# Performance work log

Measured on AMD Instinct MI355X. Metric: run time of the kernel, lower is better.

The kernel has to match this reference:

```python
import jax, jax.numpy as jnp
import numpy as np

B = 4; D = H = W = 28; C = 192; NH = 6; WS = 7; SS = 3
L = D * H * W; N = WS ** 3; HD = C // NH


def _rel_index():
    c = np.stack(np.meshgrid(np.arange(WS), np.arange(WS), np.arange(WS), indexing='ij')).reshape(3, -1)
    r = c[:, :, None] - c[:, None, :] + (WS - 1)
    return jnp.asarray(r[0] * (2 * WS - 1) ** 2 + r[1] * (2 * WS - 1) + r[2])  # (N,N)


def _attn_mask():
    img = np.zeros((D, H, W), np.float32)
    sl = (slice(0, -WS), slice(-WS, -SS), slice(-SS, None))
    cnt = 0
    for d in sl:
        for h in sl:
            for w in sl:
                img[d, h, w] = cnt; cnt += 1
    mw = img.reshape(D // WS, WS, H // WS, WS, W // WS, WS).transpose(0, 2, 4, 1, 3, 5).reshape(-1, N)
    am = mw[:, None, :] - mw[:, :, None]
    return jnp.asarray(np.where(am != 0, -100.0, 0.0).astype(np.float32))  # (nW,N,N)

REL_IDX = _rel_index()
ATTN_MASK = _attn_mask()


def _ln(x, g, b):
    m = x.mean(-1, keepdims=True)
    v = ((x - m) ** 2).mean(-1, keepdims=True)
    return (x - m) / jnp.sqrt(v + 1e-5) * g + b


def _window_partition(x):  # (B,D,H,W,C) -> (B*nW, N, C)
    x = x.reshape(B, D // WS, WS, H // WS, WS, W // WS, WS, C)
    return x.transpose(0, 1, 3, 5, 2, 4, 6, 7).reshape(-1, N, C)


def _window_reverse(w):  # (B*nW, N, C) -> (B,D,H,W,C)
    x = w.reshape(B, D // WS, H // WS, W // WS, WS, WS, WS, C)
    return x.transpose(0, 1, 4, 2, 5, 3, 6, 7).reshape(B, D, H, W, C)


def setup_inputs() -> dict:
    key = jax.random.key(0)
    ks = jax.random.split(key, 8)
    s = 0.02
    return {
        'x': jax.random.normal(ks[0], (B, L, C), jnp.float32),
        'norm1_g': jnp.ones((C,), jnp.float32), 'norm1_b': jnp.zeros((C,), jnp.float32),
        'qkv_w': jax.random.normal(ks[1], (3 * C, C), jnp.float32) * s,
        'qkv_b': jnp.zeros((3 * C,), jnp.float32),
        'proj_w': jax.random.normal(ks[2], (C, C), jnp.float32) * s,
        'proj_b': jnp.zeros((C,), jnp.float32),
        'rel_table': jax.random.normal(ks[3], ((2 * WS - 1) ** 3, NH), jnp.float32) * s,
        'norm2_g': jnp.ones((C,), jnp.float32), 'norm2_b': jnp.zeros((C,), jnp.float32),
        'fc1_w': jax.random.normal(ks[4], (4 * C, C), jnp.float32) * s,
        'fc1_b': jnp.zeros((4 * C,), jnp.float32),
        'fc2_w': jax.random.normal(ks[5], (C, 4 * C), jnp.float32) * s,
        'fc2_b': jnp.zeros((C,), jnp.float32),
    }


def reference(x, norm1_g, norm1_b, qkv_w, qkv_b, proj_w, proj_b, rel_table,
              norm2_g, norm2_b, fc1_w, fc1_b, fc2_w, fc2_b):
    shortcut = x
    h = _ln(x, norm1_g, norm1_b).reshape(B, D, H, W, C)
    h = jnp.roll(h, (-SS, -SS, -SS), axis=(1, 2, 3))
    xw = _window_partition(h)                                  # (B_, N, C)
    B_ = xw.shape[0]
    qkv = (xw @ qkv_w.T + qkv_b).reshape(B_, N, 3, NH, HD).transpose(2, 0, 3, 1, 4)
    q, k, v = qkv[0], qkv[1], qkv[2]                           # (B_, NH, N, HD)
    attn = jnp.einsum('bhnd,bhmd->bhnm', q * (HD ** -0.5), k)
    bias = rel_table[REL_IDX].transpose(2, 0, 1)               # (NH, N, N)
    attn = attn + bias[None]
    nW = ATTN_MASK.shape[0]
    attn = (attn.reshape(B, nW, NH, N, N) + ATTN_MASK[None, :, None]).reshape(B_, NH, N, N)
    attn = jax.nn.softmax(attn, axis=-1)
    out = jnp.einsum('bhnm,bhmd->bhnd', attn, v).transpose(0, 2, 1, 3).reshape(B_, N, C)
    out = out @ proj_w.T + proj_b
    h = _window_reverse(out)
    h = jnp.roll(h, (SS, SS, SS), axis=(1, 2, 3)).reshape(B, L, C)
    x = shortcut + h
    y = _ln(x, norm2_g, norm2_b)
    y = jax.nn.gelu(y @ fc1_w.T + fc1_b, approximate=False)
    return x + (y @ fc2_w.T + fc2_b)
```

## Files before the change

kernel.cpp:

```cpp
#include <hip/hip_runtime.h>

#define DEV __device__ __forceinline__

typedef __bf16 bf16x8 __attribute__((ext_vector_type(8)));
typedef float f32x4 __attribute__((ext_vector_type(4)));

DEV float bflo(unsigned int u) { union { unsigned int x; float f; } c; c.x = u << 16; return c.f; }
DEV unsigned short f2bf(float f) {
  union { float f; unsigned int u; } c; c.f = f;
  unsigned int u = c.u;
  return (unsigned short)((u + 0x7fffu + ((u >> 16) & 1u)) >> 16);
}
DEV unsigned int pkbf(float a, float b) {
  unsigned int r;
  asm("v_cvt_pk_bf16_f32 %0, %1, %2" : "=v"(r) : "v"(a), "v"(b));
  return r;
}
DEV float gelu_fast(float y) {
  float y2 = y * y;
  float z = y * fmaf(y2, 0.10294348f, 2.30220842f);
  float e = __builtin_amdgcn_exp2f(z);
  float r = __builtin_amdgcn_rcpf(e + 1.0f);
  return fmaf(-y, r, y);
}

DEV void gload16(const void* g, void* l) {
  __builtin_amdgcn_global_load_lds((const __attribute__((address_space(1))) void*)g,
                                   (__attribute__((address_space(3))) void*)l, 16, 0, 0);
}

__global__ __launch_bounds__(256) void wconv_all(const float* __restrict__ s0,
                                                 const float* __restrict__ s1,
                                                 const float* __restrict__ s2,
                                                 const float* __restrict__ s3,
                                                 unsigned short* __restrict__ dst) {
  int i = blockIdx.x * 256 + threadIdx.x;
  const float* src; int off, real;
  if (i < 122880)      { src = s0; off = i;          real = 110592; }
  else if (i < 172032) { src = s1; off = i - 122880; real = 36864; }
  else if (i < 319488) { src = s2; off = i - 172032; real = 147456; }
  else                 { src = s3; off = i - 319488; real = 147456; }
  dst[i] = (off < real) ? f2bf(src[off]) : (unsigned short)0;
}

__global__ __launch_bounds__(256) void bmt_kernel(const float* __restrict__ rel_table,
                                                  unsigned short* __restrict__ bmt4) {
  int wth = blockIdx.x;
  int wt = wth / 6, h = wth - wt * 6;
  int r = blockIdx.y;
  unsigned short* row = bmt4 + (((size_t)wth * 88 + r) * 352) * 4;
  for (int q = threadIdx.x; q < 352; q += 256) {
    int mb_q = 0, cls_q = 0;
    bool qv = q < 343;
    if (qv) {
      int ii_q = q / 49, rem_q = q - ii_q * 49;
      int jj_q = rem_q / 7, ww_q = rem_q - jj_q * 7;
      mb_q = ii_q * 169 + jj_q * 13 + ww_q;
      int cd_q = (wt & 4) ? (ii_q < 4 ? 1 : 2) : 0;
      int ch_q = (wt & 2) ? (jj_q < 4 ? 1 : 2) : 0;
      int cw_q = (wt & 1) ? (ww_q < 4 ? 1 : 2) : 0;
      cls_q = cd_q * 9 + ch_q * 3 + cw_q;
    }
    unsigned short ov[4];
#pragma unroll
    for (int i = 0; i < 4; i++) {
      int kk = 4 * r + i;
      float v;
      if (kk >= 343) v = -30000.f;
      else if (!qv) v = 0.f;
      else {
        int ii_k = kk / 49, rem_k = kk - ii_k * 49;
        int jj_k = rem_k / 7, ww_k = rem_k - jj_k * 7;
        int mb_k = ii_k * 169 + jj_k * 13 + ww_k;
        int cd_k = (wt & 4) ? (ii_k < 4 ? 1 : 2) : 0;
        int ch_k = (wt & 2) ? (jj_k < 4 ? 1 : 2) : 0;
        int cw_k = (wt & 1) ? (ww_k < 4 ? 1 : 2) : 0;
        int cls_k = cd_k * 9 + ch_k * 3 + cw_k;
        v = rel_table[(mb_q - mb_k + 1098) * 6 + h] * 1.4426950408889634f;
        if (cls_q != cls_k) v -= 144.26950408889634f;
      }
      ov[i] = f2bf(v);
    }
    unsigned int lo = (unsigned)ov[0] | ((unsigned)ov[1] << 16);
    unsigned int hi = (unsigned)ov[2] | ((unsigned)ov[3] << 16);
    *(uint2*)(row + q * 4) = make_uint2(lo, hi);
  }
}

__global__ __launch_bounds__(256) void ln_kernel(const float* __restrict__ x,
                                                 const float* __restrict__ g,
                                                 const float* __restrict__ b,
                                                 unsigned short* __restrict__ out) {
  int row = (blockIdx.x << 2) + (threadIdx.x >> 6);
  int lane = threadIdx.x & 63;
  int w_ = row / 343, n_ = row - w_ * 343;
  int bb = w_ >> 6, wrem = w_ & 63;
  int wd = wrem >> 4, wh = (wrem >> 2) & 3, ww = wrem & 3;
  int ii = n_ / 49, rem = n_ - ii * 49;
  int jj = rem / 7, kk = rem - jj * 7;
  int d = wd * 7 + ii + 3; if (d >= 28) d -= 28;
  int hh = wh * 7 + jj + 3; if (hh >= 28) hh -= 28;
  int wb = ww * 7 + kk + 3; if (wb >= 28) wb -= 28;
  const float* xr = x + ((size_t)bb * 21952 + (d * 28 + hh) * 28 + wb) * 192;
  float v0 = xr[lane], v1 = xr[lane + 64], v2 = xr[lane + 128];
  float s = v0 + v1 + v2;
  float sq = v0 * v0 + v1 * v1 + v2 * v2;
#pragma unroll
  for (int o = 32; o > 0; o >>= 1) {
    s += __shfl_xor(s, o, 64);
    sq += __shfl_xor(sq, o, 64);
  }
  float mean = s * (1.0f / 192.0f);
  float var = sq * (1.0f / 192.0f) - mean * mean;
  float rstd = rsqrtf(var + 1e-5f);
  unsigned short* orow = out + (size_t)row * 192;
  orow[lane]       = f2bf((v0 - mean) * rstd * g[lane] + b[lane]);
  orow[lane + 64]  = f2bf((v1 - mean) * rstd * g[lane + 64] + b[lane + 64]);
  orow[lane + 128] = f2bf((v2 - mean) * rstd * g[lane + 128] + b[lane + 128]);
}

__global__ __launch_bounds__(256) void gemm_qkv(
    const unsigned short* __restrict__ A, const unsigned short* __restrict__ W,
    const float* __restrict__ bias,
    unsigned short* __restrict__ oq, unsigned short* __restrict__ okk,
    unsigned short* __restrict__ ov) {
  __shared__ __align__(16) unsigned short As[2][128 * 64];
  __shared__ __align__(16) unsigned short Bs[2][128 * 64];
  const int K = 192;
  const int orig = blockIdx.x;
  const int xcd = orig & 7, off = orig >> 3;
  const int wgid = (xcd < 6 ? xcd * 429 : 2574 + (xcd - 6) * 428) + off;
  const int by = wgid / 5, bx = wgid - by * 5;
  const int bm = by << 7, bn = bx << 7;

  const int tid = threadIdx.x;
  const int lane = tid & 63;
  const int wv = tid >> 6;
  const int wr = wv >> 1, wc = wv & 1;
  const int l15 = lane & 15, l4 = lane >> 4;
  const int srow = lane >> 3;
  const int scole = ((lane & 7) ^ srow) << 3;

  f32x4 acc[4][4];
#pragma unroll
  for (int a = 0; a < 4; a++)
#pragma unroll
    for (int b2 = 0; b2 < 4; b2++) acc[a][b2] = (f32x4){0.f, 0.f, 0.f, 0.f};

  auto stage = [&](int kt, int buf) {
#pragma unroll
    for (int i = 0; i < 4; i++) {
      int c = (i << 2) + wv;
      int row = (c << 3) + srow;
      gload16(A + (size_t)(bm + row) * K + (kt << 6) + scole, &As[buf][c << 9]);
      gload16(W + (size_t)(bn + row) * K + (kt << 6) + scole, &Bs[buf][c << 9]);
    }
  };

  stage(0, 0);
  int cur = 0;
  for (int kt = 0; kt < 3; ++kt) {
    if (kt < 2) {
      stage(kt + 1, cur ^ 1);
      asm volatile("s_waitcnt vmcnt(8)" ::: "memory");
    } else {
      asm volatile("s_waitcnt vmcnt(0)" ::: "memory");
    }
    __builtin_amdgcn_s_barrier();
    __builtin_amdgcn_sched_barrier(0);
#pragma unroll
    for (int ks = 0; ks < 2; ks++) {
      bf16x8 af[4], bfr[4];
#pragma unroll
      for (int fm = 0; fm < 4; fm++) {
        int r = (wr << 6) + (fm << 4) + l15;
        int c = (ks << 2) + l4;
        af[fm] = *(const bf16x8*)(&As[cur][(r << 6) + ((c ^ (r & 7)) << 3)]);
      }
#pragma unroll
      for (int fn = 0; fn < 4; fn++) {
        int r = (wc << 6) + (fn << 4) + l15;
        int c = (ks << 2) + l4;
        bfr[fn] = *(const bf16x8*)(&Bs[cur][(r << 6) + ((c ^ (r & 7)) << 3)]);
      }
#pragma unroll
      for (int fm = 0; fm < 4; fm++)
#pragma unroll
        for (int fn = 0; fn < 4; fn++)
          acc[fm][fn] = __builtin_amdgcn_mfma_f32_16x16x32_bf16(bfr[fn], af[fm], acc[fm][fn], 0, 0, 0);
    }
    if (kt < 2) {
      __builtin_amdgcn_sched_barrier(0);
      __builtin_amdgcn_s_barrier();
      cur ^= 1;
    }
  }

#pragma unroll
  for (int fm = 0; fm < 4; fm++) {
    int gr = bm + (wr << 6) + (fm << 4) + l15;
    int w_ = gr / 343, n_ = gr - w_ * 343;
#pragma unroll
    for (int fn = 0; fn < 4; fn++) {
      int gc0 = bn + (wc << 6) + (fn << 4) + (l4 << 2);
      if (gc0 < 576) {
        float4 bv = *(const float4*)(bias + gc0);
        float v0 = acc[fm][fn][0] + bv.x, v1 = acc[fm][fn][1] + bv.y;
        float v2 = acc[fm][fn][2] + bv.z, v3 = acc[fm][fn][3] + bv.w;
        int which = gc0 / 192;
        int cc3 = gc0 - which * 192;
        int hh2 = cc3 >> 5, dd0 = cc3 & 31;
        size_t offo = ((size_t)(w_ * 6 + hh2) * 343 + n_) * 32 + dd0;
        if (which == 0) {
          const float sc = 0.17677669529663687f * 1.4426950408889634f;
          *(uint2*)(oq + offo) = make_uint2(pkbf(v0 * sc, v1 * sc), pkbf(v2 * sc, v3 * sc));
        } else if (which == 1) {
          *(uint2*)(okk + offo) = make_uint2(pkbf(v0, v1), pkbf(v2, v3));
        } else {
          *(uint2*)(ov + offo) = make_uint2(pkbf(v0, v1), pkbf(v2, v3));
        }
      }
    }
  }
}

__global__ __launch_bounds__(256, 3) void proj_mlp(
    const unsigned short* __restrict__ A,
    const unsigned short* __restrict__ Wp, const float* __restrict__ bp,
    const float* __restrict__ x,
    const float* __restrict__ g2, const float* __restrict__ b2,
    const unsigned short* __restrict__ W1, const float* __restrict__ b1,
    const unsigned short* __restrict__ W2, const float* __restrict__ b2b,
    float* __restrict__ out) {
  __shared__ __align__(16) char smem[41984];
  unsigned short* As = (unsigned short*)smem;
  unsigned short* Hs = (unsigned short*)(smem + 24576);
  float* red = (float*)(smem + 24576);

  const int tid = threadIdx.x, lane = tid & 63, wv = tid >> 6;
  const int l15 = lane & 15, l4 = lane >> 4;
  const int bm = blockIdx.x << 6;

  int orow[4];
#pragma unroll
  for (int fm = 0; fm < 4; fm++) {
    int gr = bm + (fm << 4) + l15;
    int w_ = gr / 343, n_ = gr - w_ * 343;
    int bb = w_ >> 6, wrem = w_ & 63;
    int wd = wrem >> 4, wh = (wrem >> 2) & 3, ww = wrem & 3;
    int ii = n_ / 49, rem = n_ - ii * 49;
    int jj = rem / 7, kk = rem - jj * 7;
    int d = wd * 7 + ii + 3; if (d >= 28) d -= 28;
    int hh = wh * 7 + jj + 3; if (hh >= 28) hh -= 28;
    int wb = ww * 7 + kk + 3; if (wb >= 28) wb -= 28;
    orow[fm] = ((bb * 21952 + (d * 28 + hh) * 28 + wb) * 192);
  }

#pragma unroll
  for (int i = 0; i < 6; i++) {
    int idx = (i << 8) + tid;
    int r = idx / 24, c = idx - r * 24;
    gload16(A + (size_t)(bm + r) * 192 + ((c ^ (r & 7)) << 3), As + r * 192 + (c << 3));
  }
  asm volatile("s_waitcnt vmcnt(0)" ::: "memory");
  __builtin_amdgcn_s_barrier();

  float4 xv[4][3];
#pragma unroll
  for (int fm = 0; fm < 4; fm++)
#pragma unroll
    for (int fn = 0; fn < 3; fn++) {
      int gc0 = wv * 48 + (fn << 4) + (l4 << 2);
      xv[fm][fn] = *(const float4*)(x + (size_t)orow[fm] + gc0);
    }

  f32x4 acc[4][3];
#pragma unroll
  for (int a = 0; a < 4; a++)
#pragma unroll
    for (int b_ = 0; b_ < 3; b_++) acc[a][b_] = (f32x4){0.f, 0.f, 0.f, 0.f};
#pragma unroll
  for (int ks = 0; ks < 6; ks++) {
    bf16x8 af[4], wpf[3];
#pragma unroll
    for (int fm = 0; fm < 4; fm++) {
      int r = (fm << 4) + l15;
      int ch = (ks << 2) + l4;
      af[fm] = *(const bf16x8*)(As + r * 192 + ((ch ^ (r & 7)) << 3));
    }
#pragma unroll
    for (int fn = 0; fn < 3; fn++) {
      int rr = wv * 48 + (fn << 4) + l15;
      wpf[fn] = *(const bf16x8*)(Wp + (size_t)rr * 192 + (ks << 5) + (l4 << 3));
    }
#pragma unroll
    for (int fm = 0; fm < 4; fm++)
#pragma unroll
      for (int fn = 0; fn < 3; fn++)
        acc[fm][fn] = __builtin_amdgcn_mfma_f32_16x16x32_bf16(wpf[fn], af[fm], acc[fm][fn], 0, 0, 0);
  }

  float ps[4], psq[4];
#pragma unroll
  for (int fm = 0; fm < 4; fm++) {
    float s = 0.f, sq = 0.f;
#pragma unroll
    for (int fn = 0; fn < 3; fn++) {
      int gc0 = wv * 48 + (fn << 4) + (l4 << 2);
      float4 bv = *(const float4*)(bp + gc0);
      acc[fm][fn][0] += bv.x + xv[fm][fn].x;
      acc[fm][fn][1] += bv.y + xv[fm][fn].y;
      acc[fm][fn][2] += bv.z + xv[fm][fn].z;
      acc[fm][fn][3] += bv.w + xv[fm][fn].w;
#pragma unroll
      for (int i = 0; i < 4; i++) {
        float v = acc[fm][fn][i];
        s += v; sq += v * v;
      }
    }
    ps[fm] = s; psq[fm] = sq;
  }
#pragma unroll
  for (int fm = 0; fm < 4; fm++) {
    ps[fm] += __shfl_xor(ps[fm], 16, 64);
    ps[fm] += __shfl_xor(ps[fm], 32, 64);
    psq[fm] += __shfl_xor(psq[fm], 16, 64);
    psq[fm] += __shfl_xor(psq[fm], 32, 64);
  }
  __syncthreads();
  if (l4 == 0) {
#pragma unroll
    for (int fm = 0; fm < 4; fm++) {
      int tr = (fm << 4) + l15;
      red[tr * 8 + wv] = ps[fm];
      red[tr * 8 + 4 + wv] = psq[fm];
    }
  }
  __syncthreads();
  if (tid < 64) {
    float s = red[tid * 8] + red[tid * 8 + 1] + red[tid * 8 + 2] + red[tid * 8 + 3];
    float sq = red[tid * 8 + 4] + red[tid * 8 + 5] + red[tid * 8 + 6] + red[tid * 8 + 7];
    float mean = s * (1.0f / 192.0f);
    float var = sq * (1.0f / 192.0f) - mean * mean;
    red[tid * 8] = mean;
    red[tid * 8 + 1] = rsqrtf(var + 1e-5f);
  }
  __syncthreads();
  unsigned int xnb[4][3][2];
#pragma unroll
  for (int fm = 0; fm < 4; fm++) {
    int tr = (fm << 4) + l15;
    float mean = red[tr * 8], rstd = red[tr * 8 + 1];
#pragma unroll
    for (int fn = 0; fn < 3; fn++) {
      int gc0 = wv * 48 + (fn << 4) + (l4 << 2);
      float4 gv = *(const float4*)(g2 + gc0);
      float4 b2v = *(const float4*)(b2 + gc0);
      float v0 = acc[fm][fn][0], v1 = acc[fm][fn][1];
      float v2 = acc[fm][fn][2], v3 = acc[fm][fn][3];
      xnb[fm][fn][0] = pkbf(v0, v1);
      xnb[fm][fn][1] = pkbf(v2, v3);
      float y0 = (v0 - mean) * rstd * gv.x + b2v.x;
      float y1 = (v1 - mean) * rstd * gv.y + b2v.y;
      float y2 = (v2 - mean) * rstd * gv.z + b2v.z;
      float y3 = (v3 - mean) * rstd * gv.w + b2v.w;
      int ch = gc0 >> 3;
      *(uint2*)(As + tr * 192 + ((ch ^ (tr & 7)) << 3) + (gc0 & 7)) =
          make_uint2(pkbf(y0, y1), pkbf(y2, y3));
    }
  }
  __syncthreads();

  f32x4 acc2[4][3];
#pragma unroll
  for (int a = 0; a < 4; a++)
#pragma unroll
    for (int b_ = 0; b_ < 3; b_++) acc2[a][b_] = (f32x4){0.f, 0.f, 0.f, 0.f};

  for (int cc = 0; cc < 6; cc++) {
    f32x4 acc1[4][2];
#pragma unroll
    for (int a = 0; a < 4; a++) {
      acc1[a][0] = (f32x4){0.f, 0.f, 0.f, 0.f};
      acc1[a][1] = (f32x4){0.f, 0.f, 0.f, 0.f};
    }
#pragma unroll
    for (int ks = 0; ks < 6; ks++) {
      bf16x8 af[4], w1f[2];
#pragma unroll
      for (int fm = 0; fm < 4; fm++) {
        int r = (fm << 4) + l15;
        int ch = (ks << 2) + l4;
        af[fm] = *(const bf16x8*)(As + r * 192 + ((ch ^ (r & 7)) << 3));
      }
#pragma unroll
      for (int fn = 0; fn < 2; fn++) {
        int hrow = (cc << 7) + (wv << 5) + (fn << 4) + l15;
        w1f[fn] = *(const bf16x8*)(W1 + (size_t)hrow * 192 + (ks << 5) + (l4 << 3));
      }
#pragma unroll
      for (int fm = 0; fm < 4; fm++)
#pragma unroll
        for (int fn = 0; fn < 2; fn++)
          acc1[fm][fn] = __builtin_amdgcn_mfma_f32_16x16x32_bf16(w1f[fn], af[fm], acc1[fm][fn], 0, 0, 0);
    }
    __syncthreads();
#pragma unroll
    for (int fm = 0; fm < 4; fm++) {
      int r = (fm << 4) + l15;
#pragma unroll
      for (int fn = 0; fn < 2; fn++) {
        int hc = (wv << 5) + (fn << 4) + (l4 << 2);
        float4 bv = *(const float4*)(b1 + (cc << 7) + hc);
        float g0 = gelu_fast(acc1[fm][fn][0] + bv.x);
        float g1 = gelu_fast(acc1[fm][fn][1] + bv.y);
        float g2_ = gelu_fast(acc1[fm][fn][2] + bv.z);
        float g3 = gelu_fast(acc1[fm][fn][3] + bv.w);
        *(uint2*)(Hs + r * 136 + hc) = make_uint2(pkbf(g0, g1), pkbf(g2_, g3));
      }
    }
    __syncthreads();
#pragma unroll
    for (int ks = 0; ks < 4; ks++) {
      bf16x8 hf[4], w2f[3];
#pragma unroll
      for (int fm = 0; fm < 4; fm++) {
        int r = (fm << 4) + l15;
        hf[fm] = *(const bf16x8*)(Hs + r * 136 + (ks << 5) + (l4 << 3));
      }
#pragma unroll
      for (int fn = 0; fn < 3; fn++) {
        int j = wv * 48 + (fn << 4) + l15;
        w2f[fn] = *(const bf16x8*)(W2 + (size_t)j * 768 + (cc << 7) + (ks << 5) + (l4 << 3));
      }
#pragma unroll
      for (int fm = 0; fm < 4; fm++)
#pragma unroll
        for (int fn = 0; fn < 3; fn++)
          acc2[fm][fn] = __builtin_amdgcn_mfma_f32_16x16x32_bf16(w2f[fn], hf[fm], acc2[fm][fn], 0, 0, 0);
    }
  }

#pragma unroll
  for (int fm = 0; fm < 4; fm++) {
#pragma unroll
    for (int fn = 0; fn < 3; fn++) {
      int gc0 = wv * 48 + (fn << 4) + (l4 << 2);
      float4 bv = *(const float4*)(b2b + gc0);
      float4 o;
      o.x = acc2[fm][fn][0] + bv.x + bflo(xnb[fm][fn][0] & 0xffffu);
      o.y = acc2[fm][fn][1] + bv.y + bflo(xnb[fm][fn][0] >> 16);
      o.z = acc2[fm][fn][2] + bv.z + bflo(xnb[fm][fn][1] & 0xffffu);
      o.w = acc2[fm][fn][3] + bv.w + bflo(xnb[fm][fn][1] >> 16);
      *(float4*)(out + (size_t)orow[fm] + gc0) = o;
    }
  }
}

__global__ __launch_bounds__(256) void attn_mfma(const unsigned short* __restrict__ q,
                                                 const unsigned short* __restrict__ k,
                                                 const unsigned short* __restrict__ v,
                                                 const unsigned short* __restrict__ bmt4,
                                                 unsigned short* __restrict__ out) {
  __shared__ __align__(16) unsigned short Ks[352 * 32];
  __shared__ __align__(16) unsigned short Vt[32 * 360];

  const int blk = blockIdx.x;
  const int h_ = blk >> 8;
  const int idx = blk & 255;
  const int cums[8] = {0, 108, 144, 180, 192, 228, 240, 252};
  int c = (idx >= 108) + (idx >= 144) + (idx >= 180) + (idx >= 192) +
          (idx >= 228) + (idx >= 240) + (idx >= 252);
  int r0 = idx - cums[c];
  int sh = (c & 2) ? 1 : 3, sw = (c & 1) ? 1 : 3;
  int p = ((c & 4) ? 1 : 3) * sh * sw;
  int b = r0 / p, q2 = r0 - b * p;
  int wd, wh, ww;
  if (c & 4) wd = 3; else { wd = q2 / (sh * sw); q2 -= wd * sh * sw; }
  if (c & 2) wh = 3; else { wh = q2 / sw; q2 -= wh * sw; }
  ww = (c & 1) ? 3 : q2;
  const int w_ = b * 64 + wd * 16 + wh * 4 + ww;
  const int wt = c;
  const int blkqkv = w_ * 6 + h_;

  const int t = threadIdx.x, lane = t & 63, wv = t >> 6;
  const int l15 = lane & 15, l4 = lane >> 4;
  const unsigned short* Qb = q + (size_t)blkqkv * (343 * 32);
  const unsigned short* Kb = k + (size_t)blkqkv * (343 * 32);
  const unsigned short* Vb = v + (size_t)blkqkv * (343 * 32);
  const unsigned short* bm4 = bmt4 + ((size_t)(wt * 6 + h_) * 88) * 352 * 4;

  for (int cc = t; cc < 1408; cc += 256) {
    int r = cc >> 2, ch = cc & 3;
    int swc = ch ^ ((r >> 1) & 3);
    uint4 val = make_uint4(0, 0, 0, 0);
    if (r < 343) val = *(const uint4*)(Kb + r * 32 + ch * 8);
    *(uint4*)(Ks + r * 32 + swc * 8) = val;
  }
#pragma unroll
  for (int ch = 0; ch < 4; ch++) {
    for (int n = t; n < 343; n += 256) {
      union { uint4 u4; unsigned short us[8]; } val;
      val.u4 = *(const uint4*)(Vb + n * 32 + ch * 8);
#pragma unroll
      for (int j = 0; j < 8; j++) Vt[(ch * 8 + j) * 360 + n] = val.us[j];
    }
  }
  for (int cc = t; cc < 288; cc += 256) {
    int d = cc / 9, n = 343 + (cc - d * 9);
    Vt[d * 360 + n] = 0;
  }
  __syncthreads();

  const int ksw = (l4 ^ ((l15 >> 1) & 3)) << 3;

  for (int tq = wv; tq < 22; tq += 4) {
    int qrow = tq * 16 + l15; if (qrow > 342) qrow = 342;
    bf16x8 qf = *(const bf16x8*)(Qb + qrow * 32 + l4 * 8);

    unsigned int u0[22], u1[22];
    float lsum = 0.f;
#pragma unroll
    for (int kt = 0; kt < 22; kt++) {
      bf16x8 kf = *(const bf16x8*)(Ks + (kt * 16 + l15) * 32 + ksw);
      f32x4 s = __builtin_amdgcn_mfma_f32_16x16x32_bf16(kf, qf, (f32x4){0.f, 0.f, 0.f, 0.f}, 0, 0, 0);
      const unsigned short* bp = bm4 + ((size_t)((kt << 2) + l4) * 352 + (tq << 4) + l15) * 4;
      uint2 bv = *(const uint2*)bp;
      float p0 = __builtin_amdgcn_exp2f(s[0] + bflo(bv.x & 0xffffu));
      float p1 = __builtin_amdgcn_exp2f(s[1] + bflo(bv.x >> 16));
      float p2 = __builtin_amdgcn_exp2f(s[2] + bflo(bv.y & 0xffffu));
      float p3 = __builtin_amdgcn_exp2f(s[3] + bflo(bv.y >> 16));
      lsum += (p0 + p1) + (p2 + p3);
      asm("v_cvt_pk_bf16_f32 %0, %1, %2" : "=v"(u0[kt]) : "v"(p0), "v"(p1));
      asm("v_cvt_pk_bf16_f32 %0, %1, %2" : "=v"(u1[kt]) : "v"(p2), "v"(p3));
    }
    lsum += __shfl_xor(lsum, 16, 64);
    lsum += __shfl_xor(lsum, 32, 64);
    float inv = 1.0f / lsum;

    f32x4 oacc0 = (f32x4){0.f, 0.f, 0.f, 0.f};
    f32x4 oacc1 = (f32x4){0.f, 0.f, 0.f, 0.f};
#pragma unroll
    for (int ck = 0; ck < 11; ck++) {
      unsigned int dw[4];
#pragma unroll
      for (int d = 0; d < 4; d++) {
        int src = l15 + 16 * ((d >> 1) + 2 * (l4 & 1));
        unsigned int x = __shfl((d & 1) ? u1[2 * ck] : u0[2 * ck], src, 64);
        unsigned int y = __shfl((d & 1) ? u1[2 * ck + 1] : u0[2 * ck + 1], src, 64);
        dw[d] = (l4 < 2) ? x : y;
      }
      union { unsigned int u[4]; bf16x8 v; } pc;
      pc.u[0] = dw[0]; pc.u[1] = dw[1]; pc.u[2] = dw[2]; pc.u[3] = dw[3];
      bf16x8 vf0 = *(const bf16x8*)(Vt + (size_t)l15 * 360 + ck * 32 + l4 * 8);
      bf16x8 vf1 = *(const bf16x8*)(Vt + (size_t)(16 + l15) * 360 + ck * 32 + l4 * 8);
      oacc0 = __builtin_amdgcn_mfma_f32_16x16x32_bf16(vf0, pc.v, oacc0, 0, 0, 0);
      oacc1 = __builtin_amdgcn_mfma_f32_16x16x32_bf16(vf1, pc.v, oacc1, 0, 0, 0);
    }

    int qg = tq * 16 + l15;
    if (qg < 343) {
      unsigned short* orow = out + ((size_t)w_ * 343 + qg) * 192 + h_ * 32;
      *(uint2*)(orow + (l4 << 2)) =
          make_uint2(pkbf(oacc0[0] * inv, oacc0[1] * inv), pkbf(oacc0[2] * inv, oacc0[3] * inv));
      *(uint2*)(orow + 16 + (l4 << 2)) =
          make_uint2(pkbf(oacc1[0] * inv, oacc1[1] * inv), pkbf(oacc1[2] * inv, oacc1[3] * inv));
    }
  }
}

extern "C" void kernel_launch(void* const* d_in, const int* in_sizes, int n_in,
                              void* d_out, int out_size, void* d_ws, size_t ws_size,
                              hipStream_t stream) {
  const float* x      = (const float*)d_in[0];
  const float* n1g    = (const float*)d_in[1];
  const float* n1b    = (const float*)d_in[2];
  const float* qkv_w  = (const float*)d_in[3];
  const float* qkv_b  = (const float*)d_in[4];
  const float* proj_w = (const float*)d_in[5];
  const float* proj_b = (const float*)d_in[6];
  const float* rel_t  = (const float*)d_in[7];
  const float* n2g    = (const float*)d_in[8];
  const float* n2b    = (const float*)d_in[9];
  const float* fc1_w  = (const float*)d_in[10];
  const float* fc1_b  = (const float*)d_in[11];
  const float* fc2_w  = (const float*)d_in[12];
  const float* fc2_b  = (const float*)d_in[13];

  char* ws = (char*)d_ws;
  if (ws_size < 147820032ull) return;
  unsigned short* WQKV  = (unsigned short*)(ws);
  unsigned short* WPROJ = (unsigned short*)(ws + 245760);
  unsigned short* WFC1  = (unsigned short*)(ws + 344064);
  unsigned short* WFC2  = (unsigned short*)(ws + 638976);
  unsigned short* XW    = (unsigned short*)(ws + 1032192);
  unsigned short* Q_    = (unsigned short*)(ws + 34750464);
  unsigned short* K_    = (unsigned short*)(ws + 68468736);
  unsigned short* V_    = (unsigned short*)(ws + 102187008);
  unsigned short* BMT4  = (unsigned short*)(ws + 135925248);
  float* OUT = (float*)d_out;

  wconv_all<<<2016, 256, 0, stream>>>(qkv_w, proj_w, fc1_w, fc2_w, WQKV);

  bmt_kernel<<<dim3(48, 88), 256, 0, stream>>>(rel_t, BMT4);

  ln_kernel<<<21952, 256, 0, stream>>>(x, n1g, n1b, XW);

  gemm_qkv<<<3430, 256, 0, stream>>>(XW, WQKV, qkv_b, Q_, K_, V_);

  attn_mfma<<<1536, 256, 0, stream>>>(Q_, K_, V_, BMT4, XW);

  proj_mlp<<<1372, 256, 0, stream>>>(XW, WPROJ, proj_b, x, n2g, n2b,
                                     WFC1, fc1_b, WFC2, fc2_b, OUT);
}
```

Measured before the change: 318.6 us.

## Widen MLP hidden chunk to 256, stream residual loads, add wave priority in attention

The fused proj+MLP kernel now processes the 768-wide hidden layer in three chunks of 256 instead of six chunks of 128. This halves the barrier/GELU round trips and doubles W1 fragment reuse per A-fragment load, at the cost of a larger Hs buffer (58 KB LDS) and lower launch-bounds occupancy (2 instead of 3 blocks). The residual x load is moved next to its use with a nontemporal hint, and the output store is nontemporal, to cut register pressure and cache pollution. The attention kernel wraps its MFMA/exp loops in s_setprio to favour waves issuing compute.

```diff
diff --git a/kernel.cpp b/kernel.cpp
--- a/kernel.cpp
+++ b/kernel.cpp
@@ -224,7 +224,7 @@
   }
 }
 
-__global__ __launch_bounds__(256, 3) void proj_mlp(
+__global__ __launch_bounds__(256, 2) void proj_mlp(
     const unsigned short* __restrict__ A,
     const unsigned short* __restrict__ Wp, const float* __restrict__ bp,
     const float* __restrict__ x,
@@ -232,7 +232,7 @@
     const unsigned short* __restrict__ W1, const float* __restrict__ b1,
     const unsigned short* __restrict__ W2, const float* __restrict__ b2b,
     float* __restrict__ out) {
-  __shared__ __align__(16) char smem[41984];
+  __shared__ __align__(16) char smem[58368];
   unsigned short* As = (unsigned short*)smem;
   unsigned short* Hs = (unsigned short*)(smem + 24576);
   float* red = (float*)(smem + 24576);
@@ -265,15 +265,6 @@
   asm volatile("s_waitcnt vmcnt(0)" ::: "memory");
   __builtin_amdgcn_s_barrier();
 
-  float4 xv[4][3];
-#pragma unroll
-  for (int fm = 0; fm < 4; fm++)
-#pragma unroll
-    for (int fn = 0; fn < 3; fn++) {
-      int gc0 = wv * 48 + (fn << 4) + (l4 << 2);
-      xv[fm][fn] = *(const float4*)(x + (size_t)orow[fm] + gc0);
-    }
-
   f32x4 acc[4][3];
 #pragma unroll
   for (int a = 0; a < 4; a++)
@@ -308,10 +299,11 @@
     for (int fn = 0; fn < 3; fn++) {
       int gc0 = wv * 48 + (fn << 4) + (l4 << 2);
       float4 bv = *(const float4*)(bp + gc0);
-      acc[fm][fn][0] += bv.x + xv[fm][fn].x;
-      acc[fm][fn][1] += bv.y + xv[fm][fn].y;
-      acc[fm][fn][2] += bv.z + xv[fm][fn].z;
-      acc[fm][fn][3] += bv.w + xv[fm][fn].w;
+      f32x4 xv = __builtin_nontemporal_load((const f32x4*)(x + (size_t)orow[fm] + gc0));
+      acc[fm][fn][0] += bv.x + xv[0];
+      acc[fm][fn][1] += bv.y + xv[1];
+      acc[fm][fn][2] += bv.z + xv[2];
+      acc[fm][fn][3] += bv.w + xv[3];
 #pragma unroll
       for (int i = 0; i < 4; i++) {
         float v = acc[fm][fn][i];
@@ -377,16 +369,15 @@
 #pragma unroll
     for (int b_ = 0; b_ < 3; b_++) acc2[a][b_] = (f32x4){0.f, 0.f, 0.f, 0.f};
 
-  for (int cc = 0; cc < 6; cc++) {
-    f32x4 acc1[4][2];
-#pragma unroll
-    for (int a = 0; a < 4; a++) {
-      acc1[a][0] = (f32x4){0.f, 0.f, 0.f, 0.f};
-      acc1[a][1] = (f32x4){0.f, 0.f, 0.f, 0.f};
-    }
+  for (int cc = 0; cc < 3; cc++) {
+    f32x4 acc1[4][4];
+#pragma unroll
+    for (int a = 0; a < 4; a++)
+#pragma unroll
+      for (int b_ = 0; b_ < 4; b_++) acc1[a][b_] = (f32x4){0.f, 0.f, 0.f, 0.f};
 #pragma unroll
     for (int ks = 0; ks < 6; ks++) {
-      bf16x8 af[4], w1f[2];
+      bf16x8 af[4], w1f[4];
 #pragma unroll
       for (int fm = 0; fm < 4; fm++) {
         int r = (fm << 4) + l15;
@@ -394,14 +385,14 @@
         af[fm] = *(const bf16x8*)(As + r * 192 + ((ch ^ (r & 7)) << 3));
       }
 #pragma unroll
-      for (int fn = 0; fn < 2; fn++) {
-        int hrow = (cc << 7) + (wv << 5) + (fn << 4) + l15;
+      for (int fn = 0; fn < 4; fn++) {
+        int hrow = (cc << 8) + (wv << 6) + (fn << 4) + l15;
         w1f[fn] = *(const bf16x8*)(W1 + (size_t)hrow * 192 + (ks << 5) + (l4 << 3));
       }
 #pragma unroll
       for (int fm = 0; fm < 4; fm++)
 #pragma unroll
-        for (int fn = 0; fn < 2; fn++)
+        for (int fn = 0; fn < 4; fn++)
           acc1[fm][fn] = __builtin_amdgcn_mfma_f32_16x16x32_bf16(w1f[fn], af[fm], acc1[fm][fn], 0, 0, 0);
     }
     __syncthreads();
@@ -409,29 +400,29 @@
     for (int fm = 0; fm < 4; fm++) {
       int r = (fm << 4) + l15;
 #pragma unroll
-      for (int fn = 0; fn < 2; fn++) {
-        int hc = (wv << 5) + (fn << 4) + (l4 << 2);
-        float4 bv = *(const float4*)(b1 + (cc << 7) + hc);
+      for (int fn = 0; fn < 4; fn++) {
+        int hc = (wv << 6) + (fn << 4) + (l4 << 2);
+        float4 bv = *(const float4*)(b1 + (cc << 8) + hc);
         float g0 = gelu_fast(acc1[fm][fn][0] + bv.x);
         float g1 = gelu_fast(acc1[fm][fn][1] + bv.y);
         float g2_ = gelu_fast(acc1[fm][fn][2] + bv.z);
         float g3 = gelu_fast(acc1[fm][fn][3] + bv.w);
-        *(uint2*)(Hs + r * 136 + hc) = make_uint2(pkbf(g0, g1), pkbf(g2_, g3));
+        *(uint2*)(Hs + r * 264 + hc) = make_uint2(pkbf(g0, g1), pkbf(g2_, g3));
       }
     }
     __syncthreads();
 #pragma unroll
-    for (int ks = 0; ks < 4; ks++) {
+    for (int ks = 0; ks < 8; ks++) {
       bf16x8 hf[4], w2f[3];
 #pragma unroll
       for (int fm = 0; fm < 4; fm++) {
         int r = (fm << 4) + l15;
-        hf[fm] = *(const bf16x8*)(Hs + r * 136 + (ks << 5) + (l4 << 3));
+        hf[fm] = *(const bf16x8*)(Hs + r * 264 + (ks << 5) + (l4 << 3));
       }
 #pragma unroll
       for (int fn = 0; fn < 3; fn++) {
         int j = wv * 48 + (fn << 4) + l15;
-        w2f[fn] = *(const bf16x8*)(W2 + (size_t)j * 768 + (cc << 7) + (ks << 5) + (l4 << 3));
+        w2f[fn] = *(const bf16x8*)(W2 + (size_t)j * 768 + (cc << 8) + (ks << 5) + (l4 << 3));
       }
 #pragma unroll
       for (int fm = 0; fm < 4; fm++)
@@ -447,12 +438,12 @@
     for (int fn = 0; fn < 3; fn++) {
       int gc0 = wv * 48 + (fn << 4) + (l4 << 2);
       float4 bv = *(const float4*)(b2b + gc0);
-      float4 o;
-      o.x = acc2[fm][fn][0] + bv.x + bflo(xnb[fm][fn][0] & 0xffffu);
-      o.y = acc2[fm][fn][1] + bv.y + bflo(xnb[fm][fn][0] >> 16);
-      o.z = acc2[fm][fn][2] + bv.z + bflo(xnb[fm][fn][1] & 0xffffu);
-      o.w = acc2[fm][fn][3] + bv.w + bflo(xnb[fm][fn][1] >> 16);
-      *(float4*)(out + (size_t)orow[fm] + gc0) = o;
+      f32x4 o;
+      o[0] = acc2[fm][fn][0] + bv.x + bflo(xnb[fm][fn][0] & 0xffffu);
+      o[1] = acc2[fm][fn][1] + bv.y + bflo(xnb[fm][fn][0] >> 16);
+      o[2] = acc2[fm][fn][2] + bv.z + bflo(xnb[fm][fn][1] & 0xffffu);
+      o[3] = acc2[fm][fn][3] + bv.w + bflo(xnb[fm][fn][1] >> 16);
+      __builtin_nontemporal_store(o, (f32x4*)(out + (size_t)orow[fm] + gc0));
     }
   }
 }
@@ -520,6 +511,7 @@
 
     unsigned int u0[22], u1[22];
     float lsum = 0.f;
+    __builtin_amdgcn_s_setprio(1);
 #pragma unroll
     for (int kt = 0; kt < 22; kt++) {
       bf16x8 kf = *(const bf16x8*)(Ks + (kt * 16 + l15) * 32 + ksw);
@@ -534,12 +526,14 @@
       asm("v_cvt_pk_bf16_f32 %0, %1, %2" : "=v"(u0[kt]) : "v"(p0), "v"(p1));
       asm("v_cvt_pk_bf16_f32 %0, %1, %2" : "=v"(u1[kt]) : "v"(p2), "v"(p3));
     }
+    __builtin_amdgcn_s_setprio(0);
     lsum += __shfl_xor(lsum, 16, 64);
     lsum += __shfl_xor(lsum, 32, 64);
     float inv = 1.0f / lsum;
 
     f32x4 oacc0 = (f32x4){0.f, 0.f, 0.f, 0.f};
     f32x4 oacc1 = (f32x4){0.f, 0.f, 0.f, 0.f};
+    __builtin_amdgcn_s_setprio(1);
 #pragma unroll
     for (int ck = 0; ck < 11; ck++) {
       unsigned int dw[4];
@@ -557,6 +551,7 @@
       oacc0 = __builtin_amdgcn_mfma_f32_16x16x32_bf16(vf0, pc.v, oacc0, 0, 0, 0);
       oacc1 = __builtin_amdgcn_mfma_f32_16x16x32_bf16(vf1, pc.v, oacc1, 0, 0, 0);
     }
+    __builtin_amdgcn_s_setprio(0);
 
     int qg = tq * 16 + l15;
     if (qg < 343) {
```

After: 326.8 us. +2.6%, slower.
